# Kernel optimization log

Measured on AMD Instinct MI355X. Metric: run time of the kernel, lower is better.

The kernel has to match this reference:

```python
import jax, jax.numpy as jnp
import numpy as np
from jax import lax

N_KERNELS = 10000
KS = 9
DILATIONS = (1, 2, 4, 8, 16)   # static dilation groups, 2000 kernels each
GROUP = N_KERNELS // len(DILATIONS)
BN_EPS = 1e-5


def setup_inputs() -> dict:
    key = jax.random.key(0)
    kx, kw, kb, klw = jax.random.split(key, 4)
    B, L, C, n_class = 16, 256, 3, 10
    x_enc = jax.random.normal(kx, (B, L, C), dtype=jnp.float32)
    # ROCKET kernels: normal weights, mean-centered per kernel
    W = jax.random.normal(kw, (N_KERNELS, C, KS), dtype=jnp.float32)
    W = W - W.mean(axis=(1, 2), keepdims=True)
    # ROCKET biases: uniform(-1, 1)
    b = jax.random.uniform(kb, (N_KERNELS,), dtype=jnp.float32) * 2.0 - 1.0
    gamma = jnp.ones((2 * N_KERNELS,), dtype=jnp.float32)
    beta = jnp.zeros((2 * N_KERNELS,), dtype=jnp.float32)
    linW = jax.random.normal(klw, (2 * N_KERNELS, n_class), dtype=jnp.float32) * 0.01
    linB = jnp.zeros((n_class,), dtype=jnp.float32)
    return {"x_enc": x_enc, "W": W, "b": b, "gamma": gamma, "beta": beta,
            "linW": linW, "linB": linB}


def _rocket_features(x, W, b):
    # x: [B, C, L]; W: [N_KERNELS, C, KS]; b: [N_KERNELS]
    feats = []
    dn = ("NCH", "OIH", "NCH")
    for i, d in enumerate(DILATIONS):
        w = W[i * GROUP:(i + 1) * GROUP]                       # [G, C, KS]
        bb = b[i * GROUP:(i + 1) * GROUP]                      # [G]
        y = lax.conv_general_dilated(x, w, window_strides=(1,),
                                     padding="SAME", rhs_dilation=(d,),
                                     dimension_numbers=dn)      # [B, G, L]
        y = y + bb[None, :, None]
        feats.append(y.max(axis=-1))                            # max pooling
        feats.append(jnp.where(y > 0, 1.0, 0.0).mean(axis=-1))  # PPV
    return jnp.concatenate(feats, axis=-1)                      # [B, 2*N_KERNELS]


def reference(x_enc, W, b, gamma, beta, linW, linB):
    x = jnp.transpose(x_enc, (0, 2, 1))        # [B, C, L]
    feat = _rocket_features(x, W, b)           # [B, 20000]
    # BatchNorm1d (training mode: batch statistics, biased variance)
    mu = feat.mean(axis=0)
    var = feat.var(axis=0)
    feat_n = (feat - mu) * lax.rsqrt(var + BN_EPS) * gamma + beta
    return feat_n @ linW + linB                # [B, num_class]
```

## Files before the change

kernel.cpp:

```cpp
#include <hip/hip_runtime.h>
#include <cmath>

#define NK       10000
#define GROUP    2000
#define SEQ_L    256
#define FEAT_DIM 20000
#define NBATCH   16

typedef _Float16 half8 __attribute__((ext_vector_type(8)));
typedef float    f32x4 __attribute__((ext_vector_type(4)));

__launch_bounds__(256)
__global__ void build_B(const float* __restrict__ x_enc,
                        _Float16* __restrict__ Bh_g,
                        _Float16* __restrict__ Bl_g)
{
    __shared__ __align__(16) float xp[3 * 384];
    const int gi  = blockIdx.x;
    const int b   = blockIdx.y;
    const int d   = 1 << gi;
    const int tid = threadIdx.x;

    for (int i = tid; i < 3 * 384; i += 256) xp[i] = 0.f;
    __syncthreads();
    for (int e = tid; e < SEQ_L * 3; e += 256) {
        const int t = e / 3;
        const int c = e - t * 3;
        xp[c * 384 + 64 + t] = x_enc[(b * SEQ_L + t) * 3 + c];
    }
    __syncthreads();

    const int base = (gi * NBATCH + b) * 1024;
#pragma unroll
    for (int q = 0; q < 4; ++q) {
        const int idx = q * 256 + tid;
        const int kb  = idx >> 8;
        const int t   = idx & 255;
        half8 hv, lv;
#pragma unroll
        for (int kk = 0; kk < 8; ++kk) {
            const int k2 = kb * 8 + kk;
            float v = 0.f;
            if (k2 < 27) {
                const int c  = (k2 >= 18) ? 2 : (k2 >= 9 ? 1 : 0);
                const int k9 = k2 - c * 9;
                v = xp[c * 384 + 64 + t + (k9 - 4) * d];
            }
            const _Float16 h = (_Float16)v;
            hv[kk] = h;
            lv[kk] = (_Float16)(v - (float)h);
        }
        *(half8*)&Bh_g[(base + idx) * 8] = hv;
        *(half8*)&Bl_g[(base + idx) * 8] = lv;
    }
}

__launch_bounds__(128)
__global__ void gemm_feat(const _Float16* __restrict__ Bh_g,
                          const _Float16* __restrict__ Bl_g,
                          const float* __restrict__ Wk,
                          const float* __restrict__ bias,
                          float* __restrict__ feat)
{
    const int mt  = blockIdx.x;
    const int gi  = blockIdx.y;
    const int b   = blockIdx.z;
    const int tid = threadIdx.x;
    const int l   = tid & 63;
    const int wv  = tid >> 6;
    const int kb  = l >> 4;
    const int lr  = l & 15;

    half8 ahi[4], alo[4];
#pragma unroll
    for (int tt = 0; tt < 4; ++tt) {
        const int nl = mt * 128 + wv * 64 + tt * 16 + lr;
        const int n  = gi * GROUP + (nl < GROUP ? nl : GROUP - 1);
#pragma unroll
        for (int j = 0; j < 8; ++j) {
            const int k = kb * 8 + j;
            const float w = (k < 27) ? Wk[n * 27 + k] : 0.f;
            const _Float16 h = (_Float16)w;
            ahi[tt][j] = h;
            alo[tt][j] = (_Float16)(w - (float)h);
        }
    }
    float bsv[4][4];
#pragma unroll
    for (int tt = 0; tt < 4; ++tt)
#pragma unroll
        for (int r = 0; r < 4; ++r) {
            const int nl = mt * 128 + wv * 64 + tt * 16 + kb * 4 + r;
            bsv[tt][r] = bias[gi * GROUP + (nl < GROUP ? nl : GROUP - 1)];
        }

    const _Float16* bhp = Bh_g + ((gi * NBATCH + b) * 1024 + kb * 256) * 8;
    const _Float16* blp = Bl_g + ((gi * NBATCH + b) * 1024 + kb * 256) * 8;

    float mx[4][4], cnt[4][4];
#pragma unroll
    for (int tt = 0; tt < 4; ++tt)
#pragma unroll
        for (int r = 0; r < 4; ++r) { mx[tt][r] = -INFINITY; cnt[tt][r] = 0.f; }

#pragma unroll
    for (int ch = 0; ch < 16; ++ch) {
        const int t = ch * 16 + lr;
        const half8 bh = *(const half8*)&bhp[t * 8];
        const half8 bl = *(const half8*)&blp[t * 8];
#pragma unroll
        for (int tt = 0; tt < 4; ++tt) {
            f32x4 acc = {0.f, 0.f, 0.f, 0.f};
            acc = __builtin_amdgcn_mfma_f32_16x16x32_f16(ahi[tt], bh, acc, 0, 0, 0);
            acc = __builtin_amdgcn_mfma_f32_16x16x32_f16(alo[tt], bh, acc, 0, 0, 0);
            acc = __builtin_amdgcn_mfma_f32_16x16x32_f16(ahi[tt], bl, acc, 0, 0, 0);
#pragma unroll
            for (int r = 0; r < 4; ++r) {
                const float y = acc[r] + bsv[tt][r];
                mx[tt][r]  = fmaxf(mx[tt][r], y);
                cnt[tt][r] += (y > 0.f) ? 1.f : 0.f;
            }
        }
    }

#pragma unroll
    for (int tt = 0; tt < 4; ++tt)
#pragma unroll
        for (int r = 0; r < 4; ++r) {
#pragma unroll
            for (int m = 1; m < 16; m <<= 1) {
                mx[tt][r]  = fmaxf(mx[tt][r], __shfl_xor(mx[tt][r], m));
                cnt[tt][r] += __shfl_xor(cnt[tt][r], m);
            }
        }

    if (lr == 0) {
        float* fb = feat + b * FEAT_DIM + gi * 4000;
#pragma unroll
        for (int tt = 0; tt < 4; ++tt)
#pragma unroll
            for (int r = 0; r < 4; ++r) {
                const int nl = mt * 128 + wv * 64 + tt * 16 + kb * 4 + r;
                if (nl < GROUP) {
                    fb[nl]        = mx[tt][r];
                    fb[2000 + nl] = cnt[tt][r] * (1.0f / 256.0f);
                }
            }
    }
}

__launch_bounds__(256)
__global__ void bn_gemv(const float* __restrict__ feat,
                        const float* __restrict__ gamma,
                        const float* __restrict__ beta,
                        const float* __restrict__ linW,
                        float* __restrict__ partial)
{
    __shared__ float gs[250], hs[250];
    const int sl  = blockIdx.x;
    const int f0  = sl * 250;
    const int tid = threadIdx.x;

    if (tid < 250) {
        const int f = f0 + tid;
        float s = 0.f, ss = 0.f;
#pragma unroll
        for (int b = 0; b < NBATCH; ++b) {
            const float v = feat[b * FEAT_DIM + f];
            s += v; ss += v * v;
        }
        const float mu  = s * (1.f / NBATCH);
        const float var = ss * (1.f / NBATCH) - mu * mu;
        const float gg  = gamma[f] * rsqrtf(var + 1e-5f);
        gs[tid] = gg;
        hs[tid] = beta[f] - mu * gg;
    }
    __syncthreads();

    const int bb = tid >> 4;
    const int ft = tid & 15;
    float acc[10];
#pragma unroll
    for (int c = 0; c < 10; ++c) acc[c] = 0.f;

    for (int i = ft; i < 250; i += 16) {
        const int f = f0 + i;
        const float tv = fmaf(feat[bb * FEAT_DIM + f], gs[i], hs[i]);
#pragma unroll
        for (int c = 0; c < 10; ++c) acc[c] = fmaf(tv, linW[f * 10 + c], acc[c]);
    }
#pragma unroll
    for (int c = 0; c < 10; ++c)
#pragma unroll
        for (int m = 1; m < 16; m <<= 1) acc[c] += __shfl_xor(acc[c], m);

    if (ft == 0) {
#pragma unroll
        for (int c = 0; c < 10; ++c)
            partial[(sl * NBATCH + bb) * 10 + c] = acc[c];
    }
}

__launch_bounds__(160)
__global__ void gemv_final(const float* __restrict__ partial,
                           const float* __restrict__ linB,
                           float* __restrict__ out)
{
    const int tid = threadIdx.x;
    const int c   = tid % 10;
    float s = linB[c];
#pragma unroll
    for (int sl = 0; sl < 80; ++sl) s += partial[sl * 160 + tid];
    out[tid] = s;
}

extern "C" void kernel_launch(void* const* d_in, const int* in_sizes, int n_in,
                              void* d_out, int out_size, void* d_ws, size_t ws_size,
                              hipStream_t stream) {
    const float* x     = (const float*)d_in[0];
    const float* Wk    = (const float*)d_in[1];
    const float* bias  = (const float*)d_in[2];
    const float* gamma = (const float*)d_in[3];
    const float* beta  = (const float*)d_in[4];
    const float* linW  = (const float*)d_in[5];
    const float* linB  = (const float*)d_in[6];
    float* out = (float*)d_out;

    float*    feat    = (float*)d_ws;
    float*    partial = feat + NBATCH * FEAT_DIM;
    _Float16* Bh      = (_Float16*)(partial + 80 * 160);
    _Float16* Bl      = Bh + 5 * NBATCH * 1024 * 8;

    build_B<<<dim3(5, NBATCH), 256, 0, stream>>>(x, Bh, Bl);
    gemm_feat<<<dim3(16, 5, NBATCH), 128, 0, stream>>>(Bh, Bl, Wk, bias, feat);
    bn_gemv<<<dim3(80), 256, 0, stream>>>(feat, gamma, beta, linW, partial);
    gemv_final<<<dim3(1), 160, 0, stream>>>(partial, linB, out);
}
```

Before: 36.28 us.

## Fuse im2col build into the feature GEMM and fold bias into the MFMA

Merges the build_B kernel into the GEMM kernel. Each block now rebuilds the fp16 hi/lo im2col tile in shared memory, so the global round-trip and one launch go away. The block now covers 256 kernels with 4 waves. The bias is folded into the MFMA as an extra K column multiplied by a constant 1, and the PPV count uses integers. The BN/GEMV stage uses 160 slices with linW staged in LDS, and the final reduction is split over 640 threads. The cost is redundant im2col construction per M-tile (8 blocks per batch and group) and the bias now carries fp16 split rounding.

Result: slower. 38.67 us (+6.6%).

```diff
diff --git a/kernel.cpp b/kernel.cpp
--- a/kernel.cpp
+++ b/kernel.cpp
@@ -11,15 +11,24 @@
 typedef float    f32x4 __attribute__((ext_vector_type(4)));
 
 __launch_bounds__(256)
-__global__ void build_B(const float* __restrict__ x_enc,
-                        _Float16* __restrict__ Bh_g,
-                        _Float16* __restrict__ Bl_g)
+__global__ void rocket_gemm(const float* __restrict__ x_enc,
+                            const float* __restrict__ Wk,
+                            const float* __restrict__ bias,
+                            float* __restrict__ feat)
 {
-    __shared__ __align__(16) float xp[3 * 384];
-    const int gi  = blockIdx.x;
-    const int b   = blockIdx.y;
+    __shared__ __align__(16) float    xp[3 * 384];
+    __shared__ __align__(16) _Float16 Bh[1024 * 8];
+    __shared__ __align__(16) _Float16 Bl[1024 * 8];
+
+    const int mt  = blockIdx.x;
+    const int gi  = blockIdx.y;
+    const int b   = blockIdx.z;
     const int d   = 1 << gi;
     const int tid = threadIdx.x;
+    const int l   = tid & 63;
+    const int wv  = tid >> 6;
+    const int kb  = l >> 4;
+    const int lr  = l & 15;
 
     for (int i = tid; i < 3 * 384; i += 256) xp[i] = 0.f;
     __syncthreads();
@@ -28,86 +37,65 @@
         const int c = e - t * 3;
         xp[c * 384 + 64 + t] = x_enc[(b * SEQ_L + t) * 3 + c];
     }
-    __syncthreads();
-
-    const int base = (gi * NBATCH + b) * 1024;
+
+    half8 ahi[4], alo[4];
+#pragma unroll
+    for (int tt = 0; tt < 4; ++tt) {
+        const int nl = mt * 256 + wv * 64 + tt * 16 + lr;
+        const int n  = gi * GROUP + (nl < GROUP ? nl : GROUP - 1);
+#pragma unroll
+        for (int j = 0; j < 8; ++j) {
+            const int k = kb * 8 + j;
+            float w;
+            if (k < 27)       w = Wk[n * 27 + k];
+            else if (k == 27) w = bias[n];
+            else              w = 0.f;
+            const _Float16 h = (_Float16)w;
+            ahi[tt][j] = h;
+            alo[tt][j] = (_Float16)(w - (float)h);
+        }
+    }
+
+    __syncthreads();
+
 #pragma unroll
     for (int q = 0; q < 4; ++q) {
         const int idx = q * 256 + tid;
-        const int kb  = idx >> 8;
+        const int kbb = idx >> 8;
         const int t   = idx & 255;
         half8 hv, lv;
 #pragma unroll
         for (int kk = 0; kk < 8; ++kk) {
-            const int k2 = kb * 8 + kk;
+            const int k2 = kbb * 8 + kk;
             float v = 0.f;
             if (k2 < 27) {
                 const int c  = (k2 >= 18) ? 2 : (k2 >= 9 ? 1 : 0);
                 const int k9 = k2 - c * 9;
                 v = xp[c * 384 + 64 + t + (k9 - 4) * d];
+            } else if (k2 == 27) {
+                v = 1.0f;
             }
             const _Float16 h = (_Float16)v;
             hv[kk] = h;
             lv[kk] = (_Float16)(v - (float)h);
         }
-        *(half8*)&Bh_g[(base + idx) * 8] = hv;
-        *(half8*)&Bl_g[(base + idx) * 8] = lv;
-    }
-}
-
-__launch_bounds__(128)
-__global__ void gemm_feat(const _Float16* __restrict__ Bh_g,
-                          const _Float16* __restrict__ Bl_g,
-                          const float* __restrict__ Wk,
-                          const float* __restrict__ bias,
-                          float* __restrict__ feat)
-{
-    const int mt  = blockIdx.x;
-    const int gi  = blockIdx.y;
-    const int b   = blockIdx.z;
-    const int tid = threadIdx.x;
-    const int l   = tid & 63;
-    const int wv  = tid >> 6;
-    const int kb  = l >> 4;
-    const int lr  = l & 15;
-
-    half8 ahi[4], alo[4];
-#pragma unroll
-    for (int tt = 0; tt < 4; ++tt) {
-        const int nl = mt * 128 + wv * 64 + tt * 16 + lr;
-        const int n  = gi * GROUP + (nl < GROUP ? nl : GROUP - 1);
-#pragma unroll
-        for (int j = 0; j < 8; ++j) {
-            const int k = kb * 8 + j;
-            const float w = (k < 27) ? Wk[n * 27 + k] : 0.f;
-            const _Float16 h = (_Float16)w;
-            ahi[tt][j] = h;
-            alo[tt][j] = (_Float16)(w - (float)h);
-        }
-    }
-    float bsv[4][4];
+        *(half8*)&Bh[idx * 8] = hv;
+        *(half8*)&Bl[idx * 8] = lv;
+    }
+    __syncthreads();
+
+    float mx[4][4];
+    int   cnt[4][4];
 #pragma unroll
     for (int tt = 0; tt < 4; ++tt)
 #pragma unroll
-        for (int r = 0; r < 4; ++r) {
-            const int nl = mt * 128 + wv * 64 + tt * 16 + kb * 4 + r;
-            bsv[tt][r] = bias[gi * GROUP + (nl < GROUP ? nl : GROUP - 1)];
-        }
-
-    const _Float16* bhp = Bh_g + ((gi * NBATCH + b) * 1024 + kb * 256) * 8;
-    const _Float16* blp = Bl_g + ((gi * NBATCH + b) * 1024 + kb * 256) * 8;
-
-    float mx[4][4], cnt[4][4];
-#pragma unroll
-    for (int tt = 0; tt < 4; ++tt)
-#pragma unroll
-        for (int r = 0; r < 4; ++r) { mx[tt][r] = -INFINITY; cnt[tt][r] = 0.f; }
+        for (int r = 0; r < 4; ++r) { mx[tt][r] = -INFINITY; cnt[tt][r] = 0; }
 
 #pragma unroll
     for (int ch = 0; ch < 16; ++ch) {
         const int t = ch * 16 + lr;
-        const half8 bh = *(const half8*)&bhp[t * 8];
-        const half8 bl = *(const half8*)&blp[t * 8];
+        const half8 bh = *(const half8*)&Bh[(kb * 256 + t) * 8];
+        const half8 bl = *(const half8*)&Bl[(kb * 256 + t) * 8];
 #pragma unroll
         for (int tt = 0; tt < 4; ++tt) {
             f32x4 acc = {0.f, 0.f, 0.f, 0.f};
@@ -116,9 +104,9 @@
             acc = __builtin_amdgcn_mfma_f32_16x16x32_f16(ahi[tt], bl, acc, 0, 0, 0);
 #pragma unroll
             for (int r = 0; r < 4; ++r) {
-                const float y = acc[r] + bsv[tt][r];
-                mx[tt][r]  = fmaxf(mx[tt][r], y);
-                cnt[tt][r] += (y > 0.f) ? 1.f : 0.f;
+                const float y = acc[r];
+                mx[tt][r]   = fmaxf(mx[tt][r], y);
+                cnt[tt][r] += (y > 0.f) ? 1 : 0;
             }
         }
     }
@@ -129,7 +117,7 @@
         for (int r = 0; r < 4; ++r) {
 #pragma unroll
             for (int m = 1; m < 16; m <<= 1) {
-                mx[tt][r]  = fmaxf(mx[tt][r], __shfl_xor(mx[tt][r], m));
+                mx[tt][r]   = fmaxf(mx[tt][r], __shfl_xor(mx[tt][r], m));
                 cnt[tt][r] += __shfl_xor(cnt[tt][r], m);
             }
         }
@@ -140,10 +128,10 @@
         for (int tt = 0; tt < 4; ++tt)
 #pragma unroll
             for (int r = 0; r < 4; ++r) {
-                const int nl = mt * 128 + wv * 64 + tt * 16 + kb * 4 + r;
+                const int nl = mt * 256 + wv * 64 + tt * 16 + kb * 4 + r;
                 if (nl < GROUP) {
                     fb[nl]        = mx[tt][r];
-                    fb[2000 + nl] = cnt[tt][r] * (1.0f / 256.0f);
+                    fb[2000 + nl] = (float)cnt[tt][r] * (1.0f / 256.0f);
                 }
             }
     }
@@ -156,12 +144,15 @@
                         const float* __restrict__ linW,
                         float* __restrict__ partial)
 {
-    __shared__ float gs[250], hs[250];
+    __shared__ float gs[125], hs[125];
+    __shared__ float lw[125 * 10];
     const int sl  = blockIdx.x;
-    const int f0  = sl * 250;
+    const int f0  = sl * 125;
     const int tid = threadIdx.x;
 
-    if (tid < 250) {
+    for (int i = tid; i < 1250; i += 256) lw[i] = linW[f0 * 10 + i];
+
+    if (tid < 125) {
         const int f = f0 + tid;
         float s = 0.f, ss = 0.f;
 #pragma unroll
@@ -183,11 +174,10 @@
 #pragma unroll
     for (int c = 0; c < 10; ++c) acc[c] = 0.f;
 
-    for (int i = ft; i < 250; i += 16) {
-        const int f = f0 + i;
-        const float tv = fmaf(feat[bb * FEAT_DIM + f], gs[i], hs[i]);
-#pragma unroll
-        for (int c = 0; c < 10; ++c) acc[c] = fmaf(tv, linW[f * 10 + c], acc[c]);
+    for (int i = ft; i < 125; i += 16) {
+        const float tv = fmaf(feat[bb * FEAT_DIM + f0 + i], gs[i], hs[i]);
+#pragma unroll
+        for (int c = 0; c < 10; ++c) acc[c] = fmaf(tv, lw[i * 10 + c], acc[c]);
     }
 #pragma unroll
     for (int c = 0; c < 10; ++c)
@@ -201,17 +191,22 @@
     }
 }
 
-__launch_bounds__(160)
+__launch_bounds__(640)
 __global__ void gemv_final(const float* __restrict__ partial,
                            const float* __restrict__ linB,
                            float* __restrict__ out)
 {
+    __shared__ float red[4][160];
     const int tid = threadIdx.x;
-    const int c   = tid % 10;
-    float s = linB[c];
-#pragma unroll
-    for (int sl = 0; sl < 80; ++sl) s += partial[sl * 160 + tid];
-    out[tid] = s;
+    const int q   = tid / 160;
+    const int o   = tid - q * 160;
+    float s = 0.f;
+    for (int sl = q; sl < 160; sl += 4) s += partial[sl * 160 + o];
+    red[q][o] = s;
+    __syncthreads();
+    if (tid < 160)
+        out[tid] = red[0][tid] + red[1][tid] + red[2][tid] + red[3][tid]
+                 + linB[tid % 10];
 }
 
 extern "C" void kernel_launch(void* const* d_in, const int* in_sizes, int n_in,
@@ -226,13 +221,10 @@
     const float* linB  = (const float*)d_in[6];
     float* out = (float*)d_out;
 
-    float*    feat    = (float*)d_ws;
-    float*    partial = feat + NBATCH * FEAT_DIM;
-    _Float16* Bh      = (_Float16*)(partial + 80 * 160);
-    _Float16* Bl      = Bh + 5 * NBATCH * 1024 * 8;
-
-    build_B<<<dim3(5, NBATCH), 256, 0, stream>>>(x, Bh, Bl);
-    gemm_feat<<<dim3(16, 5, NBATCH), 128, 0, stream>>>(Bh, Bl, Wk, bias, feat);
-    bn_gemv<<<dim3(80), 256, 0, stream>>>(feat, gamma, beta, linW, partial);
-    gemv_final<<<dim3(1), 160, 0, stream>>>(partial, linB, out);
-}
+    float* feat    = (float*)d_ws;
+    float* partial = feat + NBATCH * FEAT_DIM;
+
+    rocket_gemm<<<dim3(8, 5, NBATCH), 256, 0, stream>>>(x, Wk, bias, feat);
+    bn_gemv<<<dim3(160), 256, 0, stream>>>(feat, gamma, beta, linW, partial);
+    gemv_final<<<dim3(1), 640, 0, stream>>>(partial, linB, out);
+}
```
